# Kernel optimization log

Hardware: AMD Instinct MI355X
Metric: run time of the kernel (lower is better)

Reference implementation:

```python
import jax, jax.numpy as jnp
import numpy as np

N, M, D = 1024, 1024, 512


def setup_inputs() -> dict:
    key = jax.random.key(0)
    ks = jax.random.split(key, 12)
    s = 1.0 / np.sqrt(D)
    return {
        "q": jax.random.normal(ks[0], (N, D), jnp.float32),
        "k": jax.random.normal(ks[1], (M, D), jnp.float32),
        "v": jax.random.normal(ks[2], (M, D), jnp.float32),
        "mask": jax.random.randint(ks[3], (N, M), 0, 2) > 0,
        "Wq": jax.random.normal(ks[4], (D, D), jnp.float32) * s,
        "bq": jax.random.normal(ks[5], (D,), jnp.float32) * s,
        "Wk": jax.random.normal(ks[6], (D, D), jnp.float32) * s,
        "bk": jax.random.normal(ks[7], (D,), jnp.float32) * s,
        "Wv": jax.random.normal(ks[8], (D, D), jnp.float32) * s,
        "bv": jax.random.normal(ks[9], (D,), jnp.float32) * s,
        "Ww": jax.random.normal(ks[10], (D,), jnp.float32) * s,
        "bw": jax.random.normal(ks[11], (1,), jnp.float32) * s,
    }


def reference(q, k, v, mask, Wq, bq, Wk, bk, Wv, bv, Ww, bw):
    # Linear projections (torch Linear: x @ W.T + b)
    qp = q @ Wq.T + bq  # [N, D]
    kp = k @ Wk.T + bk  # [M, D]
    vp = v @ Wv.T + bv  # [M, D]
    # Bahdanau additive score: W(tanh(q_n + k_m)) -> [N, M]
    h = jnp.tanh(qp[:, None, :] + kp[None, :, :])  # [N, M, D]
    scores = jnp.einsum('nmd,d->nm', h, Ww) + bw[0]
    scores = jnp.where(mask, scores, jnp.float32(-1000000.0))
    attn = jax.nn.softmax(scores, axis=1)  # softmax over M (dim 1)
    context = jnp.einsum('nm,md->nd', attn, vp)  # [N, D]
    return context
```

## Files before the change

### kernel.cpp

```cpp
#include <hip/hip_runtime.h>
#include <hip/hip_bf16.h>
#include <float.h>


#define NROWS 1024
#define DDIM  512
#define MDIM  1024

typedef __attribute__((ext_vector_type(8))) short s8v;
typedef __attribute__((ext_vector_type(4))) float f4v;
typedef __attribute__((ext_vector_type(2))) float v2f;

__device__ __forceinline__ float bf2f(ushort h) {
    return __uint_as_float(((unsigned)h) << 16);
}
__device__ __forceinline__ ushort2 f2bf2(float a, float b) {
    __hip_bfloat162 t = __float22bfloat162_rn(float2{a, b});
    union { __hip_bfloat162 v; ushort2 u; } c; c.v = t;
    return c.u;
}
__device__ __forceinline__ void hl2(float a, float b, ushort2& h, ushort2& l) {
    h = f2bf2(a, b);
    l = f2bf2(a - bf2f(h.x), b - bf2f(h.y));
}

__device__ __forceinline__ void load_lds16(const float* g, float* l) {
    __builtin_amdgcn_global_load_lds(
        (const __attribute__((address_space(1))) void*)g,
        (__attribute__((address_space(3))) void*)l, 16, 0, 0);
}

__global__ __launch_bounds__(256) void proj_gemm(
    const float* __restrict__ q, const float* __restrict__ kk_,
    const float* __restrict__ v,
    const float* __restrict__ Wq, const float* __restrict__ bq,
    const float* __restrict__ Wk, const float* __restrict__ bk,
    const float* __restrict__ Wv, const float* __restrict__ bv,
    float* __restrict__ eq, float* __restrict__ ekT,
    ushort* __restrict__ vph, ushort* __restrict__ vpl,
    float* __restrict__ S, float CS)
{
    __shared__ ushort Ah[4096], Al[4096], Bh[4096], Bl[4096];

    const float* A; const float* B; const float* bias;
    int biasRow;
    if (blockIdx.z == 0)      { A = q;   B = Wq;  bias = bq; biasRow = 0; }
    else if (blockIdx.z == 1) { A = Wk;  B = kk_; bias = bk; biasRow = 1; }
    else                      { A = Wv;  B = v;   bias = bv; biasRow = 1; }

    const int bi = (blockIdx.z == 0) ? blockIdx.x : blockIdx.y;
    const int bj = (blockIdx.z == 0) ? blockIdx.y : blockIdx.x;

    const int t    = threadIdx.x;
    const int lane = t & 63;
    const int w    = t >> 6;
    const int lm   = lane & 15;
    const int lq   = lane >> 4;
    const int i0   = bi * 64;
    const int j0   = bj * 64;
    const int mh   = (w >> 1) * 32;
    const int nh   = (w & 1) * 32;

    if (blockIdx.z == 0) {
        const int jb = blockIdx.x * 8 + blockIdx.y;
        float4 zz = {0.f, 0.f, 0.f, 0.f};
#pragma unroll
        for (int p = 0; p < 8; ++p)
            *(float4*)&S[(size_t)jb * 8192 + (t + p * 256) * 4] = zz;
    }

    f4v acc[2][2] = {{{0.f,0.f,0.f,0.f},{0.f,0.f,0.f,0.f}},
                     {{0.f,0.f,0.f,0.f},{0.f,0.f,0.f,0.f}}};
    float4 pa[4], pb[4];

    const int sr = t >> 4, sc4 = t & 15;
#pragma unroll
    for (int p = 0; p < 4; ++p) {
        int r = sr + p * 16;
        pa[p] = *(const float4*)&A[(size_t)(i0 + r) * DDIM + sc4 * 4];
        pb[p] = *(const float4*)&B[(size_t)(j0 + r) * DDIM + sc4 * 4];
    }

    for (int kc = 0; kc < 8; ++kc) {
        __syncthreads();
#pragma unroll
        for (int p = 0; p < 4; ++p) {
            int r = sr + p * 16;
            int ad = r * 64 + (((sc4 >> 1) ^ (r & 7)) << 3) + (sc4 & 1) * 4;
            ushort2 h01, l01, h23, l23;
            hl2(pa[p].x, pa[p].y, h01, l01);
            hl2(pa[p].z, pa[p].w, h23, l23);
            ushort4 ha = {h01.x, h01.y, h23.x, h23.y};
            ushort4 la = {l01.x, l01.y, l23.x, l23.y};
            *(ushort4*)&Ah[ad] = ha;
            *(ushort4*)&Al[ad] = la;
            hl2(pb[p].x, pb[p].y, h01, l01);
            hl2(pb[p].z, pb[p].w, h23, l23);
            ushort4 hb = {h01.x, h01.y, h23.x, h23.y};
            ushort4 lb = {l01.x, l01.y, l23.x, l23.y};
            *(ushort4*)&Bh[ad] = hb;
            *(ushort4*)&Bl[ad] = lb;
        }
        __syncthreads();
        if (kc < 7) {
            const int k0 = (kc + 1) * 64;
#pragma unroll
            for (int p = 0; p < 4; ++p) {
                int r = sr + p * 16;
                pa[p] = *(const float4*)&A[(size_t)(i0 + r) * DDIM + k0 + sc4 * 4];
                pb[p] = *(const float4*)&B[(size_t)(j0 + r) * DDIM + k0 + sc4 * 4];
            }
        }
#pragma unroll
        for (int ks = 0; ks < 2; ++ks) {
            const int kb = ks * 4 + lq;
            s8v afh[2], afl[2], bfh[2], bfl[2];
#pragma unroll
            for (int g = 0; g < 2; ++g) {
                int ra = mh + g * 16 + lm;
                int rb = nh + g * 16 + lm;
                int aa = ra * 64 + ((kb ^ (ra & 7)) << 3);
                int ab = rb * 64 + ((kb ^ (rb & 7)) << 3);
                afh[g] = *(const s8v*)&Ah[aa];
                afl[g] = *(const s8v*)&Al[aa];
                bfh[g] = *(const s8v*)&Bh[ab];
                bfl[g] = *(const s8v*)&Bl[ab];
            }
#pragma unroll
            for (int mi = 0; mi < 2; ++mi)
#pragma unroll
                for (int ni = 0; ni < 2; ++ni) {
                    acc[mi][ni] = __builtin_amdgcn_mfma_f32_16x16x32_bf16(
                        afh[mi], bfh[ni], acc[mi][ni], 0, 0, 0);
                    acc[mi][ni] = __builtin_amdgcn_mfma_f32_16x16x32_bf16(
                        afh[mi], bfl[ni], acc[mi][ni], 0, 0, 0);
                    acc[mi][ni] = __builtin_amdgcn_mfma_f32_16x16x32_bf16(
                        afl[mi], bfh[ni], acc[mi][ni], 0, 0, 0);
                }
        }
    }

    const float CLAMP = 8192.0f;
#pragma unroll
    for (int mi = 0; mi < 2; ++mi) {
#pragma unroll
        for (int ni = 0; ni < 2; ++ni) {
#pragma unroll
            for (int p = 0; p < 4; ++p) {
                int row = i0 + mh + mi * 16 + lq * 4 + p;
                int col = j0 + nh + ni * 16 + lm;
                float val = acc[mi][ni][p] + (biasRow ? bias[row] : bias[col]);
                if (blockIdx.z == 0) {
                    eq[(size_t)row * 512 + col] =
                        fminf(__builtin_amdgcn_exp2f(val * CS), CLAMP);
                } else if (blockIdx.z == 1) {
                    ekT[(size_t)row * 1024 + col] =
                        fminf(__builtin_amdgcn_exp2f(val * CS), CLAMP);
                } else {
                    ushort2 h2 = f2bf2(val, val);
                    vph[(size_t)row * 1024 + col] = h2.x;
                    ushort2 l2 = f2bf2(val - bf2f(h2.x), 0.f);
                    vpl[(size_t)row * 1024 + col] = l2.x;
                }
            }
        }
    }
}

#define DCH  16
#define SMCH 128
__global__ __launch_bounds__(256) void score_kernel(const float* __restrict__ eq,
                                                    const float* __restrict__ ekT,
                                                    const float* __restrict__ Ww,
                                                    float* __restrict__ S)
{
    __shared__ __align__(16) float ks[DCH * SMCH];
    __shared__ __align__(16) float es[16 * 128];
    __shared__ __align__(16) float wws[128];
    const int t    = threadIdx.x;
    const int lane = t & 63;
    const int w    = t >> 6;
    const int m0   = blockIdx.x * SMCH;
    const int n0   = blockIdx.y * 16;
    const int dbase = blockIdx.z * 128;

    const float SC = 1.220703125e-4f;

#pragma unroll
    for (int p = 0; p < 2; ++p) {
        int idx = t + p * 256;
        int nl = idx >> 5, dd4 = idx & 31;
        float4 e4 = *(const float4*)&eq[(size_t)(n0 + nl) * DDIM + dbase + dd4 * 4];
        float4 e4s = {e4.x * SC, e4.y * SC, e4.z * SC, e4.w * SC};
        *(float4*)&es[nl * 128 + dd4 * 4] = e4s;
    }
    if (t < 128) wws[t] = Ww[dbase + t] * SC;

    v2f acc[4] = {};
    const v2f cc2 = {1.220703125e-4f, 1.220703125e-4f};

    for (int dc = 0; dc < 128; dc += DCH) {
        const int d0 = dbase + dc;
        __syncthreads();
#pragma unroll
        for (int i = 0; i < 2; ++i) {
            int r2 = w * 4 + i * 2;
            const float* g = ekT + (size_t)(d0 + r2 + (lane >> 5)) * MDIM
                             + m0 + (lane & 31) * 4;
            load_lds16(g, &ks[r2 * SMCH]);
        }
        __syncthreads();

#pragma unroll
        for (int dq = 0; dq < DCH; dq += 8) {
            v2f k0 = *(const v2f*)&ks[(dq + 0) * SMCH + lane * 2];
            v2f k1 = *(const v2f*)&ks[(dq + 1) * SMCH + lane * 2];
            v2f k2 = *(const v2f*)&ks[(dq + 2) * SMCH + lane * 2];
            v2f k3 = *(const v2f*)&ks[(dq + 3) * SMCH + lane * 2];
            v2f k4 = *(const v2f*)&ks[(dq + 4) * SMCH + lane * 2];
            v2f k5 = *(const v2f*)&ks[(dq + 5) * SMCH + lane * 2];
            v2f k6 = *(const v2f*)&ks[(dq + 6) * SMCH + lane * 2];
            v2f k7 = *(const v2f*)&ks[(dq + 7) * SMCH + lane * 2];
            float4 wgA = *(const float4*)&wws[dc + dq];
            float4 wgB = *(const float4*)&wws[dc + dq + 4];
#pragma unroll
            for (int nn = 0; nn < 4; ++nn) {
                float4 egA = *(const float4*)&es[(w * 4 + nn) * 128 + dc + dq];
                float4 egB = *(const float4*)&es[(w * 4 + nn) * 128 + dc + dq + 4];
                v2f A0 = __builtin_elementwise_fma(k0, (v2f){egA.x, egA.x}, cc2);
                v2f A1 = __builtin_elementwise_fma(k1, (v2f){egA.y, egA.y}, cc2);
                v2f A2 = __builtin_elementwise_fma(k2, (v2f){egA.z, egA.z}, cc2);
                v2f A3 = __builtin_elementwise_fma(k3, (v2f){egA.w, egA.w}, cc2);
                v2f A4 = __builtin_elementwise_fma(k4, (v2f){egB.x, egB.x}, cc2);
                v2f A5 = __builtin_elementwise_fma(k5, (v2f){egB.y, egB.y}, cc2);
                v2f A6 = __builtin_elementwise_fma(k6, (v2f){egB.z, egB.z}, cc2);
                v2f A7 = __builtin_elementwise_fma(k7, (v2f){egB.w, egB.w}, cc2);
                v2f n01 = __builtin_elementwise_fma((v2f){wgA.y, wgA.y}, A0,
                                                    (v2f){wgA.x, wgA.x} * A1);
                v2f d01 = A0 * A1;
                v2f n23 = __builtin_elementwise_fma((v2f){wgA.w, wgA.w}, A2,
                                                    (v2f){wgA.z, wgA.z} * A3);
                v2f d23 = A2 * A3;
                v2f n45 = __builtin_elementwise_fma((v2f){wgB.y, wgB.y}, A4,
                                                    (v2f){wgB.x, wgB.x} * A5);
                v2f d45 = A4 * A5;
                v2f n67 = __builtin_elementwise_fma((v2f){wgB.w, wgB.w}, A6,
                                                    (v2f){wgB.z, wgB.z} * A7);
                v2f d67 = A6 * A7;
                v2f nA = __builtin_elementwise_fma(n01, d23, n23 * d01);
                v2f dA = d01 * d23;
                v2f nB = __builtin_elementwise_fma(n45, d67, n67 * d45);
                v2f dB = d45 * d67;
                v2f num = __builtin_elementwise_fma(nA, dB, nB * dA);
                v2f den = dA * dB;
                v2f r = {__builtin_amdgcn_rcpf(den.x), __builtin_amdgcn_rcpf(den.y)};
                acc[nn] = __builtin_elementwise_fma(num, r, acc[nn]);
            }
        }
    }

    const float C2 = -2.8853900817779268f;
    const int m = m0 + lane * 2;
#pragma unroll
    for (int nn = 0; nn < 4; ++nn) {
        int n = n0 + w * 4 + nn;
        atomicAdd(&S[(size_t)n * MDIM + m],     acc[nn].x * C2);
        atomicAdd(&S[(size_t)n * MDIM + m + 1], acc[nn].y * C2);
    }
}

__global__ __launch_bounds__(256) void combine_kernel(const float* __restrict__ S,
                                                      const int* __restrict__ mask,
                                                      ushort* __restrict__ Ph,
                                                      ushort* __restrict__ Pl,
                                                      float* __restrict__ rsum)
{
    __shared__ float red[4];
    const int n = blockIdx.x, t = threadIdx.x;
    const int lane = t & 63, w = t >> 6;

    float4 s  = *(const float4*)&S[(size_t)n * MDIM + t * 4];
    int4   mk = *(const int4*)&mask[(size_t)n * MDIM + t * 4];
    float p0 = mk.x ? __builtin_amdgcn_exp2f(s.x) : 0.f;
    float p1 = mk.y ? __builtin_amdgcn_exp2f(s.y) : 0.f;
    float p2 = mk.z ? __builtin_amdgcn_exp2f(s.z) : 0.f;
    float p3 = mk.w ? __builtin_amdgcn_exp2f(s.w) : 0.f;

    ushort2 h01, l01, h23, l23;
    hl2(p0, p1, h01, l01);
    hl2(p2, p3, h23, l23);
    ushort4 hv = {h01.x, h01.y, h23.x, h23.y};
    ushort4 lv = {l01.x, l01.y, l23.x, l23.y};
    *(ushort4*)&Ph[(size_t)n * MDIM + t * 4] = hv;
    *(ushort4*)&Pl[(size_t)n * MDIM + t * 4] = lv;

    float rs = (p0 + p1) + (p2 + p3);
#pragma unroll
    for (int off = 32; off; off >>= 1) rs += __shfl_xor(rs, off);
    if (lane == 0) red[w] = rs;
    __syncthreads();
    if (t == 0) rsum[n] = (red[0] + red[1]) + (red[2] + red[3]);
}

__global__ __launch_bounds__(256) void ctx_gemm(const ushort* __restrict__ Ph,
                                                const ushort* __restrict__ Pl,
                                                const ushort* __restrict__ vph,
                                                const ushort* __restrict__ vpl,
                                                const float* __restrict__ rsum,
                                                float* __restrict__ out)
{
    const int t    = threadIdx.x;
    const int lane = t & 63;
    const int w    = t >> 6;
    const int lm   = lane & 15;
    const int lq   = lane >> 4;
    const int d0   = blockIdx.x * 64 + w * 16;
    const int n0   = blockIdx.y * 16;

    const ushort* pAh = Ph  + (size_t)(n0 + lm) * MDIM + lq * 8;
    const ushort* pAl = Pl  + (size_t)(n0 + lm) * MDIM + lq * 8;
    const ushort* pBh = vph + (size_t)(d0 + lm) * MDIM + lq * 8;
    const ushort* pBl = vpl + (size_t)(d0 + lm) * MDIM + lq * 8;

    f4v acc = {0.f, 0.f, 0.f, 0.f};
#pragma unroll 4
    for (int m0 = 0; m0 < MDIM; m0 += 32) {
        s8v ah = *(const s8v*)(pAh + m0);
        s8v al = *(const s8v*)(pAl + m0);
        s8v bh = *(const s8v*)(pBh + m0);
        s8v bl = *(const s8v*)(pBl + m0);
        acc = __builtin_amdgcn_mfma_f32_16x16x32_bf16(ah, bh, acc, 0, 0, 0);
        acc = __builtin_amdgcn_mfma_f32_16x16x32_bf16(ah, bl, acc, 0, 0, 0);
        acc = __builtin_amdgcn_mfma_f32_16x16x32_bf16(al, bh, acc, 0, 0, 0);
    }

#pragma unroll
    for (int p = 0; p < 4; ++p) {
        int nrow = n0 + lq * 4 + p;
        float inv = __builtin_amdgcn_rcpf(rsum[nrow]);
        out[(size_t)nrow * DDIM + d0 + lm] = acc[p] * inv;
    }
}

extern "C" void kernel_launch(void* const* d_in, const int* in_sizes, int n_in,
                              void* d_out, int out_size, void* d_ws, size_t ws_size,
                              hipStream_t stream)
{
    const float* q    = (const float*)d_in[0];
    const float* k    = (const float*)d_in[1];
    const float* v    = (const float*)d_in[2];
    const int*   mask = (const int*)d_in[3];
    const float* Wq   = (const float*)d_in[4];
    const float* bq   = (const float*)d_in[5];
    const float* Wk   = (const float*)d_in[6];
    const float* bk   = (const float*)d_in[7];
    const float* Wv   = (const float*)d_in[8];
    const float* bv   = (const float*)d_in[9];
    const float* Ww   = (const float*)d_in[10];

    float* ws    = (float*)d_ws;
    float* eq    = ws;
    float* ekT   = ws + 524288;
    ushort* vph  = (ushort*)(ws + 1048576);
    ushort* vpl  = (ushort*)(ws + 1310720);
    float* S     = ws + 1572864;
    float* rsum  = ws + 2621440;
    ushort* Ph   = (ushort*)ws;
    ushort* Pl   = (ushort*)(ws + 524288);
    float* out   = (float*)d_out;

    const float CS = 2.8853900817779268f;

    proj_gemm<<<dim3(16, 8, 3), dim3(256), 0, stream>>>(q, k, v, Wq, bq, Wk, bk,
                                                        Wv, bv, eq, ekT,
                                                        vph, vpl, S, CS);
    score_kernel<<<dim3(8, 64, 4), dim3(256), 0, stream>>>(eq, ekT, Ww, S);
    combine_kernel<<<dim3(1024), dim3(256), 0, stream>>>(S, mask, Ph, Pl, rsum);
    ctx_gemm<<<dim3(8, 64), dim3(256), 0, stream>>>(Ph, Pl, vph, vpl, rsum, out);
}
```

Measured before the change: 177.3 us.

## Double-buffer ekT LDS tiles in score kernel to overlap loads with compute

Halves the per-iteration d-chunk to 8 and adds a second LDS buffer for the ekT tile, prefetching the next chunk while the current one is computed. This replaces two barriers per iteration with one, and is meant to hide global-to-LDS load latency behind the rational-tanh arithmetic. The trade-off is more loop iterations, each with less work per barrier, which may limit how much latency is actually hidden.

Result: slower. 183.5 us (+3.5%).

```diff
diff --git a/kernel.cpp b/kernel.cpp
--- a/kernel.cpp
+++ b/kernel.cpp
@@ -167,14 +167,14 @@
     }
 }
 
-#define DCH  16
+#define DCH  8
 #define SMCH 128
 __global__ __launch_bounds__(256) void score_kernel(const float* __restrict__ eq,
                                                     const float* __restrict__ ekT,
                                                     const float* __restrict__ Ww,
                                                     float* __restrict__ S)
 {
-    __shared__ __align__(16) float ks[DCH * SMCH];
+    __shared__ __align__(16) float ks[2][DCH * SMCH];
     __shared__ __align__(16) float es[16 * 128];
     __shared__ __align__(16) float wws[128];
     const int t    = threadIdx.x;
@@ -196,37 +196,41 @@
     }
     if (t < 128) wws[t] = Ww[dbase + t] * SC;
 
+    {
+        const float* g = ekT + (size_t)(dbase + w * 2 + (lane >> 5)) * MDIM
+                         + m0 + (lane & 31) * 4;
+        load_lds16(g, &ks[0][(w * 2) * SMCH]);
+    }
+    __syncthreads();
+
     v2f acc[4] = {};
     const v2f cc2 = {1.220703125e-4f, 1.220703125e-4f};
+    int buf = 0;
 
     for (int dc = 0; dc < 128; dc += DCH) {
-        const int d0 = dbase + dc;
-        __syncthreads();
-#pragma unroll
-        for (int i = 0; i < 2; ++i) {
-            int r2 = w * 4 + i * 2;
-            const float* g = ekT + (size_t)(d0 + r2 + (lane >> 5)) * MDIM
-                             + m0 + (lane & 31) * 4;
-            load_lds16(g, &ks[r2 * SMCH]);
-        }
-        __syncthreads();
-
-#pragma unroll
-        for (int dq = 0; dq < DCH; dq += 8) {
-            v2f k0 = *(const v2f*)&ks[(dq + 0) * SMCH + lane * 2];
-            v2f k1 = *(const v2f*)&ks[(dq + 1) * SMCH + lane * 2];
-            v2f k2 = *(const v2f*)&ks[(dq + 2) * SMCH + lane * 2];
-            v2f k3 = *(const v2f*)&ks[(dq + 3) * SMCH + lane * 2];
-            v2f k4 = *(const v2f*)&ks[(dq + 4) * SMCH + lane * 2];
-            v2f k5 = *(const v2f*)&ks[(dq + 5) * SMCH + lane * 2];
-            v2f k6 = *(const v2f*)&ks[(dq + 6) * SMCH + lane * 2];
-            v2f k7 = *(const v2f*)&ks[(dq + 7) * SMCH + lane * 2];
-            float4 wgA = *(const float4*)&wws[dc + dq];
-            float4 wgB = *(const float4*)&wws[dc + dq + 4];
+        if (dc + DCH < 128) {
+            const float* g = ekT
+                + (size_t)(dbase + dc + DCH + w * 2 + (lane >> 5)) * MDIM
+                + m0 + (lane & 31) * 4;
+            load_lds16(g, &ks[buf ^ 1][(w * 2) * SMCH]);
+        }
+
+        {
+            const float* kb = &ks[buf][0];
+            v2f k0 = *(const v2f*)&kb[0 * SMCH + lane * 2];
+            v2f k1 = *(const v2f*)&kb[1 * SMCH + lane * 2];
+            v2f k2 = *(const v2f*)&kb[2 * SMCH + lane * 2];
+            v2f k3 = *(const v2f*)&kb[3 * SMCH + lane * 2];
+            v2f k4 = *(const v2f*)&kb[4 * SMCH + lane * 2];
+            v2f k5 = *(const v2f*)&kb[5 * SMCH + lane * 2];
+            v2f k6 = *(const v2f*)&kb[6 * SMCH + lane * 2];
+            v2f k7 = *(const v2f*)&kb[7 * SMCH + lane * 2];
+            float4 wgA = *(const float4*)&wws[dc];
+            float4 wgB = *(const float4*)&wws[dc + 4];
 #pragma unroll
             for (int nn = 0; nn < 4; ++nn) {
-                float4 egA = *(const float4*)&es[(w * 4 + nn) * 128 + dc + dq];
-                float4 egB = *(const float4*)&es[(w * 4 + nn) * 128 + dc + dq + 4];
+                float4 egA = *(const float4*)&es[(w * 4 + nn) * 128 + dc];
+                float4 egB = *(const float4*)&es[(w * 4 + nn) * 128 + dc + 4];
                 v2f A0 = __builtin_elementwise_fma(k0, (v2f){egA.x, egA.x}, cc2);
                 v2f A1 = __builtin_elementwise_fma(k1, (v2f){egA.y, egA.y}, cc2);
                 v2f A2 = __builtin_elementwise_fma(k2, (v2f){egA.z, egA.z}, cc2);
@@ -257,6 +261,9 @@
                 acc[nn] = __builtin_elementwise_fma(num, r, acc[nn]);
             }
         }
+
+        __syncthreads();
+        buf ^= 1;
     }
 
     const float C2 = -2.8853900817779268f;
```

## Register-prefetch score tiles and split ctx GEMM over M across waves

Applied to the files above, without the earlier changes.

In the score kernel, the direct global-to-LDS async loads are replaced by register prefetch: the next ekT chunk is loaded into registers while the current chunk is computed, then written to LDS between barriers. This aims to hide global load latency behind the tanh-sum arithmetic. In ctx_gemm, each block now covers 16 output columns and its four waves split the M reduction, combining partials through LDS. That gives four times more blocks for better occupancy, at the cost of an extra LDS reduction and a barrier.

Result: no change. 178.0 us (+0.4%).

```diff
diff --git a/kernel.cpp b/kernel.cpp
--- a/kernel.cpp
+++ b/kernel.cpp
@@ -22,12 +22,6 @@
 __device__ __forceinline__ void hl2(float a, float b, ushort2& h, ushort2& l) {
     h = f2bf2(a, b);
     l = f2bf2(a - bf2f(h.x), b - bf2f(h.y));
-}
-
-__device__ __forceinline__ void load_lds16(const float* g, float* l) {
-    __builtin_amdgcn_global_load_lds(
-        (const __attribute__((address_space(1))) void*)g,
-        (__attribute__((address_space(3))) void*)l, 16, 0, 0);
 }
 
 __global__ __launch_bounds__(256) void proj_gemm(
@@ -196,20 +190,25 @@
     }
     if (t < 128) wws[t] = Ww[dbase + t] * SC;
 
+    const int srow = t >> 5;
+    const int scol = (t & 31) * 4;
+    const float* gbase = ekT + (size_t)(dbase + srow) * MDIM + m0 + scol;
+
+    float4 ra = *(const float4*)(gbase);
+    float4 rb = *(const float4*)(gbase + (size_t)8 * MDIM);
+    *(float4*)&ks[srow * SMCH + scol] = ra;
+    *(float4*)&ks[(8 + srow) * SMCH + scol] = rb;
+    __syncthreads();
+
     v2f acc[4] = {};
     const v2f cc2 = {1.220703125e-4f, 1.220703125e-4f};
 
     for (int dc = 0; dc < 128; dc += DCH) {
-        const int d0 = dbase + dc;
-        __syncthreads();
-#pragma unroll
-        for (int i = 0; i < 2; ++i) {
-            int r2 = w * 4 + i * 2;
-            const float* g = ekT + (size_t)(d0 + r2 + (lane >> 5)) * MDIM
-                             + m0 + (lane & 31) * 4;
-            load_lds16(g, &ks[r2 * SMCH]);
-        }
-        __syncthreads();
+        if (dc + DCH < 128) {
+            const float* g = gbase + (size_t)(dc + DCH) * MDIM;
+            ra = *(const float4*)(g);
+            rb = *(const float4*)(g + (size_t)8 * MDIM);
+        }
 
 #pragma unroll
         for (int dq = 0; dq < DCH; dq += 8) {
@@ -257,6 +256,13 @@
                 acc[nn] = __builtin_elementwise_fma(num, r, acc[nn]);
             }
         }
+
+        __syncthreads();
+        if (dc + DCH < 128) {
+            *(float4*)&ks[srow * SMCH + scol] = ra;
+            *(float4*)&ks[(8 + srow) * SMCH + scol] = rb;
+        }
+        __syncthreads();
     }
 
     const float C2 = -2.8853900817779268f;
@@ -309,22 +315,24 @@
                                                 const float* __restrict__ rsum,
                                                 float* __restrict__ out)
 {
+    __shared__ __align__(16) float red[3 * 64 * 4];
     const int t    = threadIdx.x;
     const int lane = t & 63;
     const int w    = t >> 6;
     const int lm   = lane & 15;
     const int lq   = lane >> 4;
-    const int d0   = blockIdx.x * 64 + w * 16;
+    const int d0   = blockIdx.x * 16;
     const int n0   = blockIdx.y * 16;
-
-    const ushort* pAh = Ph  + (size_t)(n0 + lm) * MDIM + lq * 8;
-    const ushort* pAl = Pl  + (size_t)(n0 + lm) * MDIM + lq * 8;
-    const ushort* pBh = vph + (size_t)(d0 + lm) * MDIM + lq * 8;
-    const ushort* pBl = vpl + (size_t)(d0 + lm) * MDIM + lq * 8;
+    const int mb   = w * 256;
+
+    const ushort* pAh = Ph  + (size_t)(n0 + lm) * MDIM + mb + lq * 8;
+    const ushort* pAl = Pl  + (size_t)(n0 + lm) * MDIM + mb + lq * 8;
+    const ushort* pBh = vph + (size_t)(d0 + lm) * MDIM + mb + lq * 8;
+    const ushort* pBl = vpl + (size_t)(d0 + lm) * MDIM + mb + lq * 8;
 
     f4v acc = {0.f, 0.f, 0.f, 0.f};
 #pragma unroll 4
-    for (int m0 = 0; m0 < MDIM; m0 += 32) {
+    for (int m0 = 0; m0 < 256; m0 += 32) {
         s8v ah = *(const s8v*)(pAh + m0);
         s8v al = *(const s8v*)(pAl + m0);
         s8v bh = *(const s8v*)(pBh + m0);
@@ -334,11 +342,18 @@
         acc = __builtin_amdgcn_mfma_f32_16x16x32_bf16(al, bh, acc, 0, 0, 0);
     }
 
-#pragma unroll
-    for (int p = 0; p < 4; ++p) {
-        int nrow = n0 + lq * 4 + p;
-        float inv = __builtin_amdgcn_rcpf(rsum[nrow]);
-        out[(size_t)nrow * DDIM + d0 + lm] = acc[p] * inv;
+    if (w > 0) *(f4v*)&red[((w - 1) * 64 + lane) * 4] = acc;
+    __syncthreads();
+    if (w == 0) {
+#pragma unroll
+        for (int i = 0; i < 3; ++i)
+            acc += *(const f4v*)&red[(i * 64 + lane) * 4];
+#pragma unroll
+        for (int p = 0; p < 4; ++p) {
+            int nrow = n0 + lq * 4 + p;
+            float inv = __builtin_amdgcn_rcpf(rsum[nrow]);
+            out[(size_t)nrow * DDIM + d0 + lm] = acc[p] * inv;
+        }
     }
 }
 
@@ -376,5 +391,5 @@
                                                         vph, vpl, S, CS);
     score_kernel<<<dim3(8, 64, 4), dim3(256), 0, stream>>>(eq, ekT, Ww, S);
     combine_kernel<<<dim3(1024), dim3(256), 0, stream>>>(S, mask, Ph, Pl, rsum);
-    ctx_gemm<<<dim3(8, 64), dim3(256), 0, stream>>>(Ph, Pl, vph, vpl, rsum, out);
-}
+    ctx_gemm<<<dim3(32, 64), dim3(256), 0, stream>>>(Ph, Pl, vph, vpl, rsum, out);
+}
```
